# Kernel optimization log

Hardware: AMD Instinct MI355X
Metric: run time of the kernel (lower is better)

Reference implementation:

```python
import jax, jax.numpy as jnp
import numpy as np


def setup_inputs() -> dict:
    key = jax.random.key(0)
    kx, kw = jax.random.split(key)
    x = jax.random.normal(kx, (4096, 4096), dtype=jnp.float32)
    weight = jax.random.uniform(kw, (7, 7), dtype=jnp.float32)
    bias = jnp.zeros((1,), dtype=jnp.float32)
    return {"x": x, "weight": weight, "bias": bias}


def reference(x, weight, bias):
    # Valid 2D cross-correlation (stride 1, no padding) + scalar bias,
    # identical math to corr2d(X, K) + bias in the torch module.
    lhs = x[None, None, :, :]          # [N=1, C=1, H, W]
    rhs = weight[None, None, :, :]     # [O=1, I=1, kh, kw]
    y = jax.lax.conv_general_dilated(
        lhs, rhs,
        window_strides=(1, 1),
        padding='VALID',
        dimension_numbers=('NCHW', 'OIHW', 'NCHW'),
    )
    return y[0, 0] + bias[0]  # [H-kh+1, W-kw+1]
```

## Files before the change

### kernel.cpp

```cpp
#include <hip/hip_runtime.h>

#define TILE_W 128
#define TILE_H 64
#define HALO   6
#define IN_H   (TILE_H + HALO)
#define LDS_W  136
#define CPR    (LDS_W / 4)
#define TILE_CHUNKS (IN_H * CPR)
#define STAGE_INSTR ((TILE_CHUNKS + 63) / 64)
#define LDS_FLOATS  (STAGE_INSTR * 64 * 4)
#define N  4096
#define ON 4090

__device__ __forceinline__ void gload_lds16(const float* g, float* l) {
    __builtin_amdgcn_global_load_lds(
        (const __attribute__((address_space(1))) void*)g,
        (__attribute__((address_space(3))) void*)l,
        16, 0, 0);
}

__global__ __launch_bounds__(256, 4)
void conv7x7_kernel(const float* __restrict__ x,
                    const float* __restrict__ w,
                    const float* __restrict__ bias,
                    float* __restrict__ out)
{
    __shared__ float tile[LDS_FLOATS];

    const int tid  = threadIdx.x;
    const int lane = tid & 63;
    const int wv   = tid >> 6;
    const int x0   = blockIdx.x * TILE_W;
    const int y0   = blockIdx.y * TILE_H;

    {
        const int xc0 = x0 >> 2;
        for (int k = wv; k < STAGE_INSTR; k += 4) {
            const int m   = (k << 6) + lane;
            const int row = m / CPR;
            const int cc  = m - row * CPR;
            const int gy  = min(y0 + row, N - 1);
            const int gc  = min(xc0 + cc, (N >> 2) - 1);
            const float* src = x + ((size_t)gy << 12) + ((size_t)gc << 2);
            gload_lds16(src, tile + (k << 8));
        }
    }

    float ws[49];
    #pragma unroll
    for (int i = 0; i < 49; ++i) ws[i] = w[i];
    const float bv = bias[0];

    __syncthreads();

    const int tau   = tid & 31;
    const int rg    = tid >> 5;
    const int colf  = tau << 2;
    const int rbase = rg << 3;

    float acc[8][4] = {};

    #pragma unroll
    for (int rr = 0; rr < 14; ++rr) {
        const float* rp = tile + (rbase + rr) * LDS_W + colf;
        float v[10];
        const float4 a = *reinterpret_cast<const float4*>(rp);
        const float4 b = *reinterpret_cast<const float4*>(rp + 4);
        const float2 c = *reinterpret_cast<const float2*>(rp + 8);
        v[0]=a.x; v[1]=a.y; v[2]=a.z; v[3]=a.w;
        v[4]=b.x; v[5]=b.y; v[6]=b.z; v[7]=b.w;
        v[8]=c.x; v[9]=c.y;

        #pragma unroll
        for (int r = 0; r < 8; ++r) {
            const int ky = rr - r;
            if (ky >= 0 && ky < 7) {
                #pragma unroll
                for (int kx = 0; kx < 7; ++kx) {
                    const float wk = ws[ky * 7 + kx];
                    #pragma unroll
                    for (int j = 0; j < 4; ++j)
                        acc[r][j] = fmaf(v[kx + j], wk, acc[r][j]);
                }
            }
        }
    }

    const int ox  = x0 + colf;
    const int oy0 = y0 + rbase;
    if (ox + 4 <= ON && oy0 + 8 <= ON) {
        #pragma unroll
        for (int r = 0; r < 8; ++r) {
            float* dst = out + (size_t)(oy0 + r) * ON + ox;
            *reinterpret_cast<float2*>(dst)     = make_float2(acc[r][0] + bv, acc[r][1] + bv);
            *reinterpret_cast<float2*>(dst + 2) = make_float2(acc[r][2] + bv, acc[r][3] + bv);
        }
    } else {
        #pragma unroll
        for (int r = 0; r < 8; ++r) {
            const int oy = oy0 + r;
            if (oy < ON) {
                float* dst = out + (size_t)oy * ON;
                #pragma unroll
                for (int j = 0; j < 4; ++j) {
                    const int oxj = ox + j;
                    if (oxj < ON) dst[oxj] = acc[r][j] + bv;
                }
            }
        }
    }
}

extern "C" void kernel_launch(void* const* d_in, const int* in_sizes, int n_in,
                              void* d_out, int out_size, void* d_ws, size_t ws_size,
                              hipStream_t stream) {
    const float* x    = (const float*)d_in[0];
    const float* w    = (const float*)d_in[1];
    const float* bias = (const float*)d_in[2];
    float* out        = (float*)d_out;

    dim3 grid((ON + TILE_W - 1) / TILE_W, (ON + TILE_H - 1) / TILE_H);
    conv7x7_kernel<<<grid, dim3(256, 1, 1), 0, stream>>>(x, w, bias, out);
}
```

Baseline: 37.14 us.

## Replace LDS-staged tiles with direct global loads in 7x7 convolution

Removes the global-to-LDS staging and the block barrier, so each thread reads its 14 input rows straight from global memory. Block tiling changes from 128x64 to 64 wide by 128 tall, and the launch bound is raised to target more resident waves. The intent is to drop LDS traffic and synchronisation and rely on L1/L2 caching for halo reuse. The cost is redundant global reads of the overlapping rows between thread groups and extra cache pressure.

After: 48.95 us. 1.32x slower.

```diff
diff --git a/kernel.cpp b/kernel.cpp
--- a/kernel.cpp
+++ b/kernel.cpp
@@ -1,72 +1,41 @@
 #include <hip/hip_runtime.h>
 
-#define TILE_W 128
-#define TILE_H 64
-#define HALO   6
-#define IN_H   (TILE_H + HALO)
-#define LDS_W  136
-#define CPR    (LDS_W / 4)
-#define TILE_CHUNKS (IN_H * CPR)
-#define STAGE_INSTR ((TILE_CHUNKS + 63) / 64)
-#define LDS_FLOATS  (STAGE_INSTR * 64 * 4)
 #define N  4096
 #define ON 4090
+#define NN (N * N)
 
-__device__ __forceinline__ void gload_lds16(const float* g, float* l) {
-    __builtin_amdgcn_global_load_lds(
-        (const __attribute__((address_space(1))) void*)g,
-        (__attribute__((address_space(3))) void*)l,
-        16, 0, 0);
-}
-
-__global__ __launch_bounds__(256, 4)
-void conv7x7_kernel(const float* __restrict__ x,
+__global__ __launch_bounds__(256, 8)
+void conv7x7_direct(const float* __restrict__ x,
                     const float* __restrict__ w,
                     const float* __restrict__ bias,
                     float* __restrict__ out)
 {
-    __shared__ float tile[LDS_FLOATS];
-
-    const int tid  = threadIdx.x;
-    const int lane = tid & 63;
-    const int wv   = tid >> 6;
-    const int x0   = blockIdx.x * TILE_W;
-    const int y0   = blockIdx.y * TILE_H;
-
-    {
-        const int xc0 = x0 >> 2;
-        for (int k = wv; k < STAGE_INSTR; k += 4) {
-            const int m   = (k << 6) + lane;
-            const int row = m / CPR;
-            const int cc  = m - row * CPR;
-            const int gy  = min(y0 + row, N - 1);
-            const int gc  = min(xc0 + cc, (N >> 2) - 1);
-            const float* src = x + ((size_t)gy << 12) + ((size_t)gc << 2);
-            gload_lds16(src, tile + (k << 8));
-        }
-    }
+    const int tid = threadIdx.x;
+    const int tau = tid & 15;
+    const int rg  = tid >> 4;
+    const int x0  = blockIdx.x * 64;
+    const int y0  = blockIdx.y * 128;
+    const int ox  = x0 + (tau << 2);
+    const int oy0 = y0 + (rg << 3);
 
     float ws[49];
     #pragma unroll
     for (int i = 0; i < 49; ++i) ws[i] = w[i];
     const float bv = bias[0];
 
-    __syncthreads();
-
-    const int tau   = tid & 31;
-    const int rg    = tid >> 5;
-    const int colf  = tau << 2;
-    const int rbase = rg << 3;
-
     float acc[8][4] = {};
 
     #pragma unroll
     for (int rr = 0; rr < 14; ++rr) {
-        const float* rp = tile + (rbase + rr) * LDS_W + colf;
+        const int gy = min(oy0 + rr, N - 1);
+        const int lb = (gy << 12) + ox;
+        const int l1 = min(lb + 4, NN - 4);
+        const int l2 = min(lb + 8, NN - 2);
+
         float v[10];
-        const float4 a = *reinterpret_cast<const float4*>(rp);
-        const float4 b = *reinterpret_cast<const float4*>(rp + 4);
-        const float2 c = *reinterpret_cast<const float2*>(rp + 8);
+        const float4 a = *reinterpret_cast<const float4*>(x + lb);
+        const float4 b = *reinterpret_cast<const float4*>(x + l1);
+        const float2 c = *reinterpret_cast<const float2*>(x + l2);
         v[0]=a.x; v[1]=a.y; v[2]=a.z; v[3]=a.w;
         v[4]=b.x; v[5]=b.y; v[6]=b.z; v[7]=b.w;
         v[8]=c.x; v[9]=c.y;
@@ -86,8 +55,6 @@
         }
     }
 
-    const int ox  = x0 + colf;
-    const int oy0 = y0 + rbase;
     if (ox + 4 <= ON && oy0 + 8 <= ON) {
         #pragma unroll
         for (int r = 0; r < 8; ++r) {
@@ -119,6 +86,6 @@
     const float* bias = (const float*)d_in[2];
     float* out        = (float*)d_out;
 
-    dim3 grid((ON + TILE_W - 1) / TILE_W, (ON + TILE_H - 1) / TILE_H);
-    conv7x7_kernel<<<grid, dim3(256, 1, 1), 0, stream>>>(x, w, bias, out);
+    dim3 grid((ON + 63) / 64, (ON + 127) / 128);
+    conv7x7_direct<<<grid, dim3(256, 1, 1), 0, stream>>>(x, w, bias, out);
 }
```
